# Performance work log

Measured on AMD Instinct MI355X. Metric: run time of the kernel, lower is better.

The kernel has to match this reference:

```python
import jax, jax.numpy as jnp
import numpy as np

B, T, HID = 2, 2048, 1024
NH, HD = 16, 64          # attn_heads, head_size (NH*HD == HID)
FF = 4 * HID
LN_EPS = 1e-5            # torch nn.LayerNorm default


def setup_inputs() -> dict:
    key = jax.random.key(0)
    ks = jax.random.split(key, 14)
    s = lambda fan_in: fan_in ** -0.5
    return {
        "embedding": jax.random.normal(ks[0], (B, T, HID), jnp.float32),
        # per-head q/k/v projections stacked: [HID, NH, HD] (no bias, as in torch code)
        "Wq": jax.random.normal(ks[1], (HID, NH, HD), jnp.float32) * s(HID),
        "Wk": jax.random.normal(ks[2], (HID, NH, HD), jnp.float32) * s(HID),
        "Wv": jax.random.normal(ks[3], (HID, NH, HD), jnp.float32) * s(HID),
        "Wo": jax.random.normal(ks[4], (HID, HID), jnp.float32) * s(HID),
        "W1": jax.random.normal(ks[5], (HID, FF), jnp.float32) * s(HID),
        "b1": jnp.zeros((FF,), jnp.float32),
        "W2": jax.random.normal(ks[6], (FF, HID), jnp.float32) * s(FF),
        "b2": jnp.zeros((HID,), jnp.float32),
        "g1": jnp.ones((HID,), jnp.float32),
        "be1": jnp.zeros((HID,), jnp.float32),
        "g2": jnp.ones((HID,), jnp.float32),
        "be2": jnp.zeros((HID,), jnp.float32),
    }


def _layer_norm(h, g, b):
    mu = jnp.mean(h, axis=-1, keepdims=True)
    var = jnp.mean(jnp.square(h - mu), axis=-1, keepdims=True)
    return (h - mu) * jax.lax.rsqrt(var + LN_EPS) * g + b


def _block(x, Wq, Wk, Wv, Wo, W1, b1, W2, b2, g1, be1, g2, be2):
    # --- causal multi-head self-attention (pre-LN) ---
    h = _layer_norm(x, g1, be1)
    q = jnp.einsum('btd,dhk->bhtk', h, Wq)
    k = jnp.einsum('btd,dhk->bhtk', h, Wk)
    v = jnp.einsum('btd,dhk->bhtk', h, Wv)
    scores = jnp.einsum('bhtk,bhsk->bhts', q, k) * (HD ** -0.5)
    causal = jnp.tril(jnp.ones((T, T), bool))
    scores = jnp.where(causal, scores, -jnp.inf)
    attn = jax.nn.softmax(scores, axis=-1)
    ctx = jnp.einsum('bhts,bhsk->bhtk', attn, v)          # [B,NH,T,HD]
    ctx = ctx.transpose(0, 2, 1, 3).reshape(x.shape[0], x.shape[1], HID)
    x = x + ctx @ Wo
    # --- feed-forward (pre-LN) ---
    h2 = _layer_norm(x, g2, be2)
    ff = jax.nn.relu(h2 @ W1 + b1) @ W2 + b2
    return x + ff


def reference(embedding, Wq, Wk, Wv, Wo, W1, b1, W2, b2, g1, be1, g2, be2):
    return _block(embedding, Wq, Wk, Wv, Wo, W1, b1, W2, b2, g1, be1, g2, be2)
```

## Files before the change

kernel.cpp:

```cpp
#include <hip/hip_runtime.h>
#include <math.h>

#define HIDDEN 1024
#define SEQ    2048
#define NHEAD  16
#define HDIM   64
#define ROWS   (2 * SEQ)

typedef float  floatx4  __attribute__((ext_vector_type(4)));
typedef float  floatx16 __attribute__((ext_vector_type(16)));
typedef __bf16 bf16x8   __attribute__((ext_vector_type(8)));
typedef __bf16 bf16x4   __attribute__((ext_vector_type(4)));

#define AS1(p) ((const __attribute__((address_space(1))) void*)(p))
#define AS3(p) ((__attribute__((address_space(3))) void*)(p))

#define SWZ(row, chunk) ((((chunk) ^ ((row) & 7)) * 8))

__global__ __launch_bounds__(256) void ln_kernel(const float* __restrict__ x,
                                                 const float* __restrict__ g,
                                                 const float* __restrict__ beta,
                                                 __bf16* __restrict__ out) {
    int row = blockIdx.x;
    int tid = threadIdx.x;
    const float* xr = x + (size_t)row * HIDDEN;
    float4 v = *(const float4*)(xr + tid * 4);
    float s  = v.x + v.y + v.z + v.w;
    float s2 = v.x * v.x + v.y * v.y + v.z * v.z + v.w * v.w;
#pragma unroll
    for (int off = 1; off < 64; off <<= 1) {
        s  += __shfl_xor(s, off, 64);
        s2 += __shfl_xor(s2, off, 64);
    }
    __shared__ float red[8];
    int wid = tid >> 6;
    if ((tid & 63) == 0) { red[wid] = s; red[wid + 4] = s2; }
    __syncthreads();
    s  = red[0] + red[1] + red[2] + red[3];
    s2 = red[4] + red[5] + red[6] + red[7];
    float mu  = s * (1.0f / HIDDEN);
    float var = fmaxf(s2 * (1.0f / HIDDEN) - mu * mu, 0.0f);
    float inv = rsqrtf(var + 1e-5f);
    float4 gv = *(const float4*)(g + tid * 4);
    float4 bv = *(const float4*)(beta + tid * 4);
    bf16x4 o;
    o[0] = (__bf16)((v.x - mu) * inv * gv.x + bv.x);
    o[1] = (__bf16)((v.y - mu) * inv * gv.y + bv.y);
    o[2] = (__bf16)((v.z - mu) * inv * gv.z + bv.z);
    o[3] = (__bf16)((v.w - mu) * inv * gv.w + bv.w);
    *(bf16x4*)(out + (size_t)row * HIDDEN + tid * 4) = o;
}

__global__ __launch_bounds__(256) void red_wo_ln(const float* __restrict__ emb,
                                                 const __bf16* __restrict__ p0,
                                                 const __bf16* __restrict__ p1,
                                                 const float* __restrict__ g,
                                                 const float* __restrict__ beta,
                                                 float* __restrict__ out,
                                                 __bf16* __restrict__ h2) {
    int row = blockIdx.x;
    int tid = threadIdx.x;
    size_t i = (size_t)row * HIDDEN + tid * 4;
    float4 e = *(const float4*)(emb + i);
    bf16x4 a = *(const bf16x4*)(p0 + i);
    bf16x4 b = *(const bf16x4*)(p1 + i);
    float4 v;
    v.x = e.x + (float)a[0] + (float)b[0];
    v.y = e.y + (float)a[1] + (float)b[1];
    v.z = e.z + (float)a[2] + (float)b[2];
    v.w = e.w + (float)a[3] + (float)b[3];
    *(float4*)(out + i) = v;

    float s  = v.x + v.y + v.z + v.w;
    float s2 = v.x * v.x + v.y * v.y + v.z * v.z + v.w * v.w;
#pragma unroll
    for (int off = 1; off < 64; off <<= 1) {
        s  += __shfl_xor(s, off, 64);
        s2 += __shfl_xor(s2, off, 64);
    }
    __shared__ float red[8];
    int wid = tid >> 6;
    if ((tid & 63) == 0) { red[wid] = s; red[wid + 4] = s2; }
    __syncthreads();
    s  = red[0] + red[1] + red[2] + red[3];
    s2 = red[4] + red[5] + red[6] + red[7];
    float mu  = s * (1.0f / HIDDEN);
    float var = fmaxf(s2 * (1.0f / HIDDEN) - mu * mu, 0.0f);
    float inv = rsqrtf(var + 1e-5f);
    float4 gv = *(const float4*)(g + tid * 4);
    float4 bv = *(const float4*)(beta + tid * 4);
    bf16x4 o;
    o[0] = (__bf16)((v.x - mu) * inv * gv.x + bv.x);
    o[1] = (__bf16)((v.y - mu) * inv * gv.y + bv.y);
    o[2] = (__bf16)((v.z - mu) * inv * gv.z + bv.z);
    o[3] = (__bf16)((v.w - mu) * inv * gv.w + bv.w);
    *(bf16x4*)(h2 + i) = o;
}

__global__ __launch_bounds__(256) void convt_all(const float* __restrict__ Wq,
                                                 const float* __restrict__ Wk,
                                                 const float* __restrict__ Wv,
                                                 const float* __restrict__ Wo,
                                                 const float* __restrict__ W1,
                                                 const float* __restrict__ W2,
                                                 __bf16* __restrict__ BtQKV,
                                                 __bf16* __restrict__ BtO,
                                                 __bf16* __restrict__ Bt1,
                                                 __bf16* __restrict__ Bt2) {
    __shared__ float t[32][33];
    int id = blockIdx.x;
    const float* in; __bf16* out; int K, N, nt, kt;
    if (id < 4096) {
        int job = id >> 10, tt = id & 1023;
        nt = tt & 31; kt = tt >> 5; K = 1024; N = 1024;
        if (job == 0)      { in = Wq; out = BtQKV; }
        else if (job == 1) { in = Wk; out = BtQKV + 1024 * 1024; }
        else if (job == 2) { in = Wv; out = BtQKV + 2 * 1024 * 1024; }
        else               { in = Wo; out = BtO; }
    } else if (id < 8192) {
        int tt = id - 4096;
        nt = tt & 127; kt = tt >> 7; K = 1024; N = 4096; in = W1; out = Bt1;
    } else {
        int tt = id - 8192;
        nt = tt & 31; kt = tt >> 5; K = 4096; N = 1024; in = W2; out = Bt2;
    }
    int n0 = nt * 32, k0 = kt * 32;
    int r  = threadIdx.x >> 3;
    int c4 = (threadIdx.x & 7) * 4;
    float4 v = *(const float4*)(in + (size_t)(k0 + r) * N + n0 + c4);
    t[r][c4 + 0] = v.x; t[r][c4 + 1] = v.y; t[r][c4 + 2] = v.z; t[r][c4 + 3] = v.w;
    __syncthreads();
    bf16x4 o;
    o[0] = (__bf16)t[c4 + 0][r];
    o[1] = (__bf16)t[c4 + 1][r];
    o[2] = (__bf16)t[c4 + 2][r];
    o[3] = (__bf16)t[c4 + 3][r];
    *(bf16x4*)(out + (size_t)(n0 + r) * K + k0 + c4) = o;
}

__device__ __forceinline__ void mfma_core128(const __bf16* __restrict__ A,
                                             const __bf16* __restrict__ Bt,
                                             int Kstride, int Klen,
                                             int m0, int n0, int tid,
                                             floatx16 (&acc)[2][2]) {
    __shared__ __bf16 As[128 * 32];
    __shared__ __bf16 Bs[128 * 32];
    int lane = tid & 63;
    int wave = tid >> 6;
    int wr = wave >> 1, wc = wave & 1;

    int sr = lane >> 2;
    int sk = 8 * ((lane & 3) ^ ((sr >> 1) & 3));
    const __bf16* ga0 = A  + (size_t)(m0 + wave * 16 + sr) * Kstride + sk;
    const __bf16* ga1 = ga0 + (size_t)64 * Kstride;
    const __bf16* gb0 = Bt + (size_t)(n0 + wave * 16 + sr) * Kstride + sk;
    const __bf16* gb1 = gb0 + (size_t)64 * Kstride;
    __bf16* la0 = &As[wave * 512];
    __bf16* la1 = &As[2048 + wave * 512];
    __bf16* lb0 = &Bs[wave * 512];
    __bf16* lb1 = &Bs[2048 + wave * 512];

    int fm = lane & 31;
    int gswz = (lane >> 1) & 3;
    int slot0 = ((lane >> 5) + 0) ^ gswz;
    int slot1 = ((lane >> 5) + 2) ^ gswz;

    for (int k0 = 0; k0 < Klen; k0 += 32) {
        __builtin_amdgcn_global_load_lds(AS1(ga0 + k0), AS3(la0), 16, 0, 0);
        __builtin_amdgcn_global_load_lds(AS1(ga1 + k0), AS3(la1), 16, 0, 0);
        __builtin_amdgcn_global_load_lds(AS1(gb0 + k0), AS3(lb0), 16, 0, 0);
        __builtin_amdgcn_global_load_lds(AS1(gb1 + k0), AS3(lb1), 16, 0, 0);
        __syncthreads();

        bf16x8 af[2][2], bfv[2][2];
#pragma unroll
        for (int i = 0; i < 2; i++) {
            const __bf16* rp = As + (size_t)(wr * 64 + i * 32 + fm) * 32;
            af[i][0] = *(const bf16x8*)(rp + slot0 * 8);
            af[i][1] = *(const bf16x8*)(rp + slot1 * 8);
        }
#pragma unroll
        for (int j = 0; j < 2; j++) {
            const __bf16* rp = Bs + (size_t)(wc * 64 + j * 32 + fm) * 32;
            bfv[j][0] = *(const bf16x8*)(rp + slot0 * 8);
            bfv[j][1] = *(const bf16x8*)(rp + slot1 * 8);
        }
#pragma unroll
        for (int t = 0; t < 2; t++)
#pragma unroll
            for (int i = 0; i < 2; i++)
#pragma unroll
                for (int j = 0; j < 2; j++)
                    acc[i][j] = __builtin_amdgcn_mfma_f32_32x32x16_bf16(
                        af[i][t], bfv[j][t], acc[i][j], 0, 0, 0);
        __syncthreads();
    }
}

template <typename OutT, bool BIAS, bool RELU, bool RES>
__global__ __launch_bounds__(256) void mgemm(const __bf16* __restrict__ A,
                                             const __bf16* __restrict__ Bt,
                                             const float* __restrict__ bias,
                                             const float* __restrict__ res,
                                             OutT* __restrict__ C,
                                             int M, int N, int Kstride, int Klen) {
    int tid = threadIdx.x;
    int lane = tid & 63;
    int wave = tid >> 6;
    int m0 = blockIdx.x * 128, n0 = blockIdx.y * 128;
    int wr = wave >> 1, wc = wave & 1;
    floatx16 acc[2][2] = {};
    mfma_core128(A, Bt, Kstride, Klen, m0, n0, tid, acc);

#pragma unroll
    for (int i = 0; i < 2; i++) {
#pragma unroll
        for (int j = 0; j < 2; j++) {
            int col  = n0 + wc * 64 + j * 32 + (lane & 31);
            int rowb = m0 + wr * 64 + i * 32 + 4 * (lane >> 5);
#pragma unroll
            for (int reg = 0; reg < 16; reg++) {
                int row = rowb + (reg & 3) + 8 * (reg >> 2);
                float v = acc[i][j][reg];
                if (BIAS) v += bias[col];
                if (RELU) v = fmaxf(v, 0.0f);
                if (RES)  v += res[(size_t)row * N + col];
                C[(size_t)row * N + col] = (OutT)v;
            }
        }
    }
}

__global__ __launch_bounds__(256) void mgemm_sk(const __bf16* __restrict__ A,
                                                const __bf16* __restrict__ Bt,
                                                __bf16* __restrict__ P0,
                                                __bf16* __restrict__ P3,
                                                int M, int N, int Kstride, int Klen) {
    int z = blockIdx.z;
    const __bf16* Az  = A  + (size_t)z * Klen;
    const __bf16* Btz = Bt + (size_t)z * Klen;
    __bf16* C = (z == 3) ? P3 : (P0 + (size_t)z * M * N);

    int tid = threadIdx.x;
    int lane = tid & 63;
    int wave = tid >> 6;
    int m0 = blockIdx.x * 128, n0 = blockIdx.y * 128;
    int wr = wave >> 1, wc = wave & 1;
    floatx16 acc[2][2] = {};
    mfma_core128(Az, Btz, Kstride, Klen, m0, n0, tid, acc);

#pragma unroll
    for (int i = 0; i < 2; i++) {
#pragma unroll
        for (int j = 0; j < 2; j++) {
            int col  = n0 + wc * 64 + j * 32 + (lane & 31);
            int rowb = m0 + wr * 64 + i * 32 + 4 * (lane >> 5);
#pragma unroll
            for (int reg = 0; reg < 16; reg++) {
                int row = rowb + (reg & 3) + 8 * (reg >> 2);
                C[(size_t)row * N + col] = (__bf16)acc[i][j][reg];
            }
        }
    }
}

__global__ __launch_bounds__(256) void red_w2(const __bf16* __restrict__ p0,
                                              const __bf16* __restrict__ p3,
                                              const float* __restrict__ b2,
                                              float* __restrict__ out,
                                              int N) {
    size_t i = ((size_t)blockIdx.x * 256 + threadIdx.x) * 8;
    const size_t MN = (size_t)ROWS * HIDDEN;
    bf16x8 a = *(const bf16x8*)(p0 + i);
    bf16x8 b = *(const bf16x8*)(p0 + MN + i);
    bf16x8 c = *(const bf16x8*)(p0 + 2 * MN + i);
    bf16x8 d = *(const bf16x8*)(p3 + i);
    int col = (int)(i & (size_t)(N - 1));
    float4 bb0 = *(const float4*)(b2 + col);
    float4 bb1 = *(const float4*)(b2 + col + 4);
    float4 o0 = *(const float4*)(out + i);
    float4 o1 = *(const float4*)(out + i + 4);
    o0.x += (float)a[0] + (float)b[0] + (float)c[0] + (float)d[0] + bb0.x;
    o0.y += (float)a[1] + (float)b[1] + (float)c[1] + (float)d[1] + bb0.y;
    o0.z += (float)a[2] + (float)b[2] + (float)c[2] + (float)d[2] + bb0.z;
    o0.w += (float)a[3] + (float)b[3] + (float)c[3] + (float)d[3] + bb0.w;
    o1.x += (float)a[4] + (float)b[4] + (float)c[4] + (float)d[4] + bb1.x;
    o1.y += (float)a[5] + (float)b[5] + (float)c[5] + (float)d[5] + bb1.y;
    o1.z += (float)a[6] + (float)b[6] + (float)c[6] + (float)d[6] + bb1.z;
    o1.w += (float)a[7] + (float)b[7] + (float)c[7] + (float)d[7] + bb1.w;
    *(float4*)(out + i)     = o0;
    *(float4*)(out + i + 4) = o1;
}

__global__ __launch_bounds__(256) void vtrans(const __bf16* __restrict__ qkv,
                                              __bf16* __restrict__ Vt) {
    __shared__ __bf16 t[64 * 64];
    int bh = blockIdx.x, b = bh >> 4, h = bh & 15;
    int t0 = blockIdx.y * 64;
    int tid = threadIdx.x;
    int lt = tid >> 2;
    int ds = (tid & 3) * 16;
    const __bf16* vp = qkv + (size_t)(b * SEQ + t0 + lt) * (3 * HIDDEN)
                     + 2 * HIDDEN + h * HDIM + ds;
    bf16x8 a = *(const bf16x8*)vp;
    bf16x8 c = *(const bf16x8*)(vp + 8);
#pragma unroll
    for (int i = 0; i < 8; i++) {
        int d0 = ds + i, d1 = ds + 8 + i;
        t[d0 * 64 + SWZ(d0, lt >> 3) + (lt & 7)] = a[i];
        t[d1 * 64 + SWZ(d1, lt >> 3) + (lt & 7)] = c[i];
    }
    __syncthreads();
    int dr = tid >> 2;
    int c2 = (tid & 3) * 2;
    bf16x8 o0 = *(const bf16x8*)&t[dr * 64 + SWZ(dr, c2)];
    bf16x8 o1 = *(const bf16x8*)&t[dr * 64 + SWZ(dr, c2 + 1)];
    __bf16* op = Vt + ((size_t)bh * HDIM + dr) * SEQ + t0;
    *(bf16x8*)(op + c2 * 8)     = o0;
    *(bf16x8*)(op + c2 * 8 + 8) = o1;
}

__global__ __launch_bounds__(256) void attn_mfma(const __bf16* __restrict__ qkv,
                                                 const __bf16* __restrict__ Vt,
                                                 __bf16* __restrict__ ctx) {
    __shared__ __bf16 Ks[64 * 64];
    __shared__ __bf16 Vs[64 * 64];
    __shared__ __bf16 Ps[4][16 * 64];
    const int QKVW = 3 * HIDDEN;

    int bh = blockIdx.x;
    int qt = gridDim.y - 1 - blockIdx.y;
    int b = bh >> 4, h = bh & 15;
    int tid = threadIdx.x;
    int lane = tid & 63;
    int w = tid >> 6;
    int m = lane & 15;
    int g = lane >> 4;

    const float QSC = 1.44269504f / 8.0f;
    bf16x8 qf[2];
    {
        const __bf16* Qp = qkv + (size_t)(b * SEQ + qt * 64 + w * 16 + m) * QKVW
                         + h * HDIM + g * 8;
        qf[0] = *(const bf16x8*)(Qp);
        qf[1] = *(const bf16x8*)(Qp + 32);
#pragma unroll
        for (int t = 0; t < 2; t++)
#pragma unroll
            for (int i = 0; i < 8; i++)
                qf[t][i] = (__bf16)((float)qf[t][i] * QSC);
    }

    bf16x8 onesf;
#pragma unroll
    for (int i = 0; i < 8; i++) onesf[i] = (__bf16)1.0f;

    floatx4 oacc[4] = {};
    floatx4 lacc = {};

    int srow = tid >> 2;
    int sc0  = (tid & 3) * 2;
    const __bf16* Kg = qkv + (size_t)(b * SEQ) * QKVW + HIDDEN + h * HDIM;
    const __bf16* Vg = Vt + (size_t)bh * HDIM * SEQ;

    for (int kt = 0; kt <= qt; kt++) {
        __syncthreads();
        {
            const __bf16* kp = Kg + (size_t)(kt * 64 + srow) * QKVW + sc0 * 8;
            bf16x8 k0 = *(const bf16x8*)kp;
            bf16x8 k1 = *(const bf16x8*)(kp + 8);
            const __bf16* vp = Vg + (size_t)srow * SEQ + kt * 64 + sc0 * 8;
            bf16x8 v0 = *(const bf16x8*)vp;
            bf16x8 v1 = *(const bf16x8*)(vp + 8);
            *(bf16x8*)&Ks[srow * 64 + SWZ(srow, sc0)]     = k0;
            *(bf16x8*)&Ks[srow * 64 + SWZ(srow, sc0 + 1)] = k1;
            *(bf16x8*)&Vs[srow * 64 + SWZ(srow, sc0)]     = v0;
            *(bf16x8*)&Vs[srow * 64 + SWZ(srow, sc0 + 1)] = v1;
        }
        __syncthreads();

        floatx4 sacc[4] = {};
#pragma unroll
        for (int j = 0; j < 4; j++) {
#pragma unroll
            for (int t = 0; t < 2; t++) {
                int kr = 16 * j + m;
                bf16x8 kf = *(const bf16x8*)&Ks[kr * 64 + SWZ(kr, g + 4 * t)];
                sacc[j] = __builtin_amdgcn_mfma_f32_16x16x32_bf16(
                    qf[t], kf, sacc[j], 0, 0, 0);
            }
        }

        if (kt == qt) {
            int qlocal = w * 16 + 4 * g;
#pragma unroll
            for (int j = 0; j < 4; j++)
#pragma unroll
                for (int r = 0; r < 4; r++)
                    if (16 * j + m > qlocal + r) sacc[j][r] = -INFINITY;
        }

        __bf16* Pw = &Ps[w][0];
#pragma unroll
        for (int j = 0; j < 4; j++)
#pragma unroll
            for (int r = 0; r < 4; r++) {
                float p = exp2f(sacc[j][r]);
                int row = 4 * g + r;
                int key = 16 * j + m;
                Pw[row * 64 + SWZ(row, key >> 3) + (key & 7)] = (__bf16)p;
            }

#pragma unroll
        for (int t = 0; t < 2; t++) {
            bf16x8 pf = *(const bf16x8*)&Pw[m * 64 + SWZ(m, g + 4 * t)];
            lacc = __builtin_amdgcn_mfma_f32_16x16x32_bf16(pf, onesf, lacc, 0, 0, 0);
#pragma unroll
            for (int jd = 0; jd < 4; jd++) {
                int vr = 16 * jd + m;
                bf16x8 vf = *(const bf16x8*)&Vs[vr * 64 + SWZ(vr, g + 4 * t)];
                oacc[jd] = __builtin_amdgcn_mfma_f32_16x16x32_bf16(
                    pf, vf, oacc[jd], 0, 0, 0);
            }
        }
    }

#pragma unroll
    for (int r = 0; r < 4; r++) {
        float invl = 1.0f / lacc[r];
        int row = qt * 64 + w * 16 + 4 * g + r;
        __bf16* cp = ctx + (size_t)(b * SEQ + row) * HIDDEN + h * HDIM;
#pragma unroll
        for (int jd = 0; jd < 4; jd++)
            cp[16 * jd + m] = (__bf16)(oacc[jd][r] * invl);
    }
}

extern "C" void kernel_launch(void* const* d_in, const int* in_sizes, int n_in,
                              void* d_out, int out_size, void* d_ws, size_t ws_size,
                              hipStream_t stream) {
    (void)in_sizes; (void)n_in; (void)out_size; (void)ws_size;
    const float* emb = (const float*)d_in[0];
    const float* Wq  = (const float*)d_in[1];
    const float* Wk  = (const float*)d_in[2];
    const float* Wv  = (const float*)d_in[3];
    const float* Wo  = (const float*)d_in[4];
    const float* W1  = (const float*)d_in[5];
    const float* b1  = (const float*)d_in[6];
    const float* W2  = (const float*)d_in[7];
    const float* b2  = (const float*)d_in[8];
    const float* g1  = (const float*)d_in[9];
    const float* be1 = (const float*)d_in[10];
    const float* g2  = (const float*)d_in[11];
    const float* be2 = (const float*)d_in[12];
    float* out = (float*)d_out;

    __bf16* wsb = (__bf16*)d_ws;
    const size_t ME = 1024 * 1024;
    __bf16* h     = wsb;
    __bf16* qkv   = wsb + 4 * ME;
    __bf16* ctx   = wsb;
    __bf16* ff1   = wsb;
    __bf16* h2    = wsb + 16 * ME;
    __bf16* BtQKV = wsb + 20 * ME;
    __bf16* BtO   = wsb + 23 * ME;
    __bf16* Bt1   = wsb + 24 * ME;
    __bf16* Bt2   = wsb + 28 * ME;
    __bf16* Vt    = wsb + 32 * ME;
    __bf16* woP   = wsb + 4 * ME;
    __bf16* w2P0  = wsb + 16 * ME;
    __bf16* w2P3  = wsb + 32 * ME;

    convt_all<<<12288, 256, 0, stream>>>(Wq, Wk, Wv, Wo, W1, W2,
                                         BtQKV, BtO, Bt1, Bt2);

    ln_kernel<<<ROWS, 256, 0, stream>>>(emb, g1, be1, h);

    mgemm<__bf16, false, false, false><<<dim3(32, 24), 256, 0, stream>>>(
        h, BtQKV, nullptr, nullptr, qkv, ROWS, 3072, 1024, 1024);

    vtrans<<<dim3(32, 32), 256, 0, stream>>>(qkv, Vt);

    attn_mfma<<<dim3(32, 32), 256, 0, stream>>>(qkv, Vt, ctx);

    mgemm_sk<<<dim3(32, 8, 2), 256, 0, stream>>>(
        ctx, BtO, woP, nullptr, ROWS, 1024, 1024, 512);
    red_wo_ln<<<ROWS, 256, 0, stream>>>(emb, woP, woP + 4 * ME, g2, be2, out, h2);

    mgemm<__bf16, true, true, false><<<dim3(32, 32), 256, 0, stream>>>(
        h2, Bt1, b1, nullptr, ff1, ROWS, 4096, 1024, 1024);

    mgemm_sk<<<dim3(32, 8, 4), 256, 0, stream>>>(
        ff1, Bt2, w2P0, w2P3, ROWS, 1024, 4096, 1024);
    red_w2<<<2048, 256, 0, stream>>>(w2P0, w2P3, b2, out, 1024);
}
```

Before: 357.2 us.

## Fuse prep kernels, double-buffer GEMM LDS, fuse V transpose, prefetch attention tiles

Merges the weight convert/transpose and first LayerNorm into one launch. Double-buffers the shared GEMM mainloop so the next K tile's global-to-LDS load overlaps the current MFMAs, with one barrier per iteration instead of two. Writes V transposed straight from the QKV GEMM epilogue, removing the separate vtrans kernel, and has attention register-prefetch the next K/V tile. The trade-offs are twice the LDS use in the GEMM (lower occupancy) and strided small stores for the V columns.

```diff
diff --git a/kernel.cpp b/kernel.cpp
--- a/kernel.cpp
+++ b/kernel.cpp
@@ -17,38 +17,80 @@
 
 #define SWZ(row, chunk) ((((chunk) ^ ((row) & 7)) * 8))
 
-__global__ __launch_bounds__(256) void ln_kernel(const float* __restrict__ x,
-                                                 const float* __restrict__ g,
-                                                 const float* __restrict__ beta,
-                                                 __bf16* __restrict__ out) {
-    int row = blockIdx.x;
+__global__ __launch_bounds__(256) void prep_all(const float* __restrict__ Wq,
+                                                const float* __restrict__ Wk,
+                                                const float* __restrict__ Wv,
+                                                const float* __restrict__ Wo,
+                                                const float* __restrict__ W1,
+                                                const float* __restrict__ W2,
+                                                __bf16* __restrict__ BtQKV,
+                                                __bf16* __restrict__ BtO,
+                                                __bf16* __restrict__ Bt1,
+                                                __bf16* __restrict__ Bt2,
+                                                const float* __restrict__ emb,
+                                                const float* __restrict__ g1,
+                                                const float* __restrict__ be1,
+                                                __bf16* __restrict__ h) {
+    int id = blockIdx.x;
     int tid = threadIdx.x;
-    const float* xr = x + (size_t)row * HIDDEN;
-    float4 v = *(const float4*)(xr + tid * 4);
-    float s  = v.x + v.y + v.z + v.w;
-    float s2 = v.x * v.x + v.y * v.y + v.z * v.z + v.w * v.w;
-#pragma unroll
-    for (int off = 1; off < 64; off <<= 1) {
-        s  += __shfl_xor(s, off, 64);
-        s2 += __shfl_xor(s2, off, 64);
-    }
-    __shared__ float red[8];
-    int wid = tid >> 6;
-    if ((tid & 63) == 0) { red[wid] = s; red[wid + 4] = s2; }
+    if (id >= 12288) {
+        int row = id - 12288;
+        const float* xr = emb + (size_t)row * HIDDEN;
+        float4 v = *(const float4*)(xr + tid * 4);
+        float s  = v.x + v.y + v.z + v.w;
+        float s2 = v.x * v.x + v.y * v.y + v.z * v.z + v.w * v.w;
+#pragma unroll
+        for (int off = 1; off < 64; off <<= 1) {
+            s  += __shfl_xor(s, off, 64);
+            s2 += __shfl_xor(s2, off, 64);
+        }
+        __shared__ float red[8];
+        int wid = tid >> 6;
+        if ((tid & 63) == 0) { red[wid] = s; red[wid + 4] = s2; }
+        __syncthreads();
+        s  = red[0] + red[1] + red[2] + red[3];
+        s2 = red[4] + red[5] + red[6] + red[7];
+        float mu  = s * (1.0f / HIDDEN);
+        float var = fmaxf(s2 * (1.0f / HIDDEN) - mu * mu, 0.0f);
+        float inv = rsqrtf(var + 1e-5f);
+        float4 gv = *(const float4*)(g1 + tid * 4);
+        float4 bv = *(const float4*)(be1 + tid * 4);
+        bf16x4 o;
+        o[0] = (__bf16)((v.x - mu) * inv * gv.x + bv.x);
+        o[1] = (__bf16)((v.y - mu) * inv * gv.y + bv.y);
+        o[2] = (__bf16)((v.z - mu) * inv * gv.z + bv.z);
+        o[3] = (__bf16)((v.w - mu) * inv * gv.w + bv.w);
+        *(bf16x4*)(h + (size_t)row * HIDDEN + tid * 4) = o;
+        return;
+    }
+    __shared__ float t[32][33];
+    const float* in; __bf16* out; int K, N, nt, kt;
+    if (id < 4096) {
+        int job = id >> 10, tt = id & 1023;
+        nt = tt & 31; kt = tt >> 5; K = 1024; N = 1024;
+        if (job == 0)      { in = Wq; out = BtQKV; }
+        else if (job == 1) { in = Wk; out = BtQKV + 1024 * 1024; }
+        else if (job == 2) { in = Wv; out = BtQKV + 2 * 1024 * 1024; }
+        else               { in = Wo; out = BtO; }
+    } else if (id < 8192) {
+        int tt = id - 4096;
+        nt = tt & 127; kt = tt >> 7; K = 1024; N = 4096; in = W1; out = Bt1;
+    } else {
+        int tt = id - 8192;
+        nt = tt & 31; kt = tt >> 5; K = 4096; N = 1024; in = W2; out = Bt2;
+    }
+    int n0 = nt * 32, k0 = kt * 32;
+    int r  = tid >> 3;
+    int c4 = (tid & 7) * 4;
+    float4 v = *(const float4*)(in + (size_t)(k0 + r) * N + n0 + c4);
+    t[r][c4 + 0] = v.x; t[r][c4 + 1] = v.y; t[r][c4 + 2] = v.z; t[r][c4 + 3] = v.w;
     __syncthreads();
-    s  = red[0] + red[1] + red[2] + red[3];
-    s2 = red[4] + red[5] + red[6] + red[7];
-    float mu  = s * (1.0f / HIDDEN);
-    float var = fmaxf(s2 * (1.0f / HIDDEN) - mu * mu, 0.0f);
-    float inv = rsqrtf(var + 1e-5f);
-    float4 gv = *(const float4*)(g + tid * 4);
-    float4 bv = *(const float4*)(beta + tid * 4);
     bf16x4 o;
-    o[0] = (__bf16)((v.x - mu) * inv * gv.x + bv.x);
-    o[1] = (__bf16)((v.y - mu) * inv * gv.y + bv.y);
-    o[2] = (__bf16)((v.z - mu) * inv * gv.z + bv.z);
-    o[3] = (__bf16)((v.w - mu) * inv * gv.w + bv.w);
-    *(bf16x4*)(out + (size_t)row * HIDDEN + tid * 4) = o;
+    o[0] = (__bf16)t[c4 + 0][r];
+    o[1] = (__bf16)t[c4 + 1][r];
+    o[2] = (__bf16)t[c4 + 2][r];
+    o[3] = (__bf16)t[c4 + 3][r];
+    *(bf16x4*)(out + (size_t)(n0 + r) * K + k0 + c4) = o;
 }
 
 __global__ __launch_bounds__(256) void red_wo_ln(const float* __restrict__ emb,
@@ -97,54 +139,14 @@
     *(bf16x4*)(h2 + i) = o;
 }
 
-__global__ __launch_bounds__(256) void convt_all(const float* __restrict__ Wq,
-                                                 const float* __restrict__ Wk,
-                                                 const float* __restrict__ Wv,
-                                                 const float* __restrict__ Wo,
-                                                 const float* __restrict__ W1,
-                                                 const float* __restrict__ W2,
-                                                 __bf16* __restrict__ BtQKV,
-                                                 __bf16* __restrict__ BtO,
-                                                 __bf16* __restrict__ Bt1,
-                                                 __bf16* __restrict__ Bt2) {
-    __shared__ float t[32][33];
-    int id = blockIdx.x;
-    const float* in; __bf16* out; int K, N, nt, kt;
-    if (id < 4096) {
-        int job = id >> 10, tt = id & 1023;
-        nt = tt & 31; kt = tt >> 5; K = 1024; N = 1024;
-        if (job == 0)      { in = Wq; out = BtQKV; }
-        else if (job == 1) { in = Wk; out = BtQKV + 1024 * 1024; }
-        else if (job == 2) { in = Wv; out = BtQKV + 2 * 1024 * 1024; }
-        else               { in = Wo; out = BtO; }
-    } else if (id < 8192) {
-        int tt = id - 4096;
-        nt = tt & 127; kt = tt >> 7; K = 1024; N = 4096; in = W1; out = Bt1;
-    } else {
-        int tt = id - 8192;
-        nt = tt & 31; kt = tt >> 5; K = 4096; N = 1024; in = W2; out = Bt2;
-    }
-    int n0 = nt * 32, k0 = kt * 32;
-    int r  = threadIdx.x >> 3;
-    int c4 = (threadIdx.x & 7) * 4;
-    float4 v = *(const float4*)(in + (size_t)(k0 + r) * N + n0 + c4);
-    t[r][c4 + 0] = v.x; t[r][c4 + 1] = v.y; t[r][c4 + 2] = v.z; t[r][c4 + 3] = v.w;
-    __syncthreads();
-    bf16x4 o;
-    o[0] = (__bf16)t[c4 + 0][r];
-    o[1] = (__bf16)t[c4 + 1][r];
-    o[2] = (__bf16)t[c4 + 2][r];
-    o[3] = (__bf16)t[c4 + 3][r];
-    *(bf16x4*)(out + (size_t)(n0 + r) * K + k0 + c4) = o;
-}
-
 __device__ __forceinline__ void mfma_core128(const __bf16* __restrict__ A,
                                              const __bf16* __restrict__ Bt,
                                              int Kstride, int Klen,
                                              int m0, int n0, int tid,
                                              floatx16 (&acc)[2][2]) {
-    __shared__ __bf16 As[128 * 32];
-    __shared__ __bf16 Bs[128 * 32];
+    __shared__ __bf16 As[2 * 128 * 32];
+    __shared__ __bf16 Bs[2 * 128 * 32];
+    const int BUF = 128 * 32;
     int lane = tid & 63;
     int wave = tid >> 6;
     int wr = wave >> 1, wc = wave & 1;
@@ -165,23 +167,34 @@
     int slot0 = ((lane >> 5) + 0) ^ gswz;
     int slot1 = ((lane >> 5) + 2) ^ gswz;
 
-    for (int k0 = 0; k0 < Klen; k0 += 32) {
-        __builtin_amdgcn_global_load_lds(AS1(ga0 + k0), AS3(la0), 16, 0, 0);
-        __builtin_amdgcn_global_load_lds(AS1(ga1 + k0), AS3(la1), 16, 0, 0);
-        __builtin_amdgcn_global_load_lds(AS1(gb0 + k0), AS3(lb0), 16, 0, 0);
-        __builtin_amdgcn_global_load_lds(AS1(gb1 + k0), AS3(lb1), 16, 0, 0);
+    __builtin_amdgcn_global_load_lds(AS1(ga0), AS3(la0), 16, 0, 0);
+    __builtin_amdgcn_global_load_lds(AS1(ga1), AS3(la1), 16, 0, 0);
+    __builtin_amdgcn_global_load_lds(AS1(gb0), AS3(lb0), 16, 0, 0);
+    __builtin_amdgcn_global_load_lds(AS1(gb1), AS3(lb1), 16, 0, 0);
+
+    int buf = 0;
+    for (int k0 = 0; k0 < Klen; k0 += 32, buf ^= 1) {
         __syncthreads();
+        if (k0 + 32 < Klen) {
+            int nb = (buf ^ 1) * BUF;
+            __builtin_amdgcn_global_load_lds(AS1(ga0 + k0 + 32), AS3(la0 + nb), 16, 0, 0);
+            __builtin_amdgcn_global_load_lds(AS1(ga1 + k0 + 32), AS3(la1 + nb), 16, 0, 0);
+            __builtin_amdgcn_global_load_lds(AS1(gb0 + k0 + 32), AS3(lb0 + nb), 16, 0, 0);
+            __builtin_amdgcn_global_load_lds(AS1(gb1 + k0 + 32), AS3(lb1 + nb), 16, 0, 0);
+        }
+        const __bf16* Ab = As + buf * BUF;
+        const __bf16* Bb = Bs + buf * BUF;
 
         bf16x8 af[2][2], bfv[2][2];
 #pragma unroll
         for (int i = 0; i < 2; i++) {
-            const __bf16* rp = As + (size_t)(wr * 64 + i * 32 + fm) * 32;
+            const __bf16* rp = Ab + (size_t)(wr * 64 + i * 32 + fm) * 32;
             af[i][0] = *(const bf16x8*)(rp + slot0 * 8);
             af[i][1] = *(const bf16x8*)(rp + slot1 * 8);
         }
 #pragma unroll
         for (int j = 0; j < 2; j++) {
-            const __bf16* rp = Bs + (size_t)(wc * 64 + j * 32 + fm) * 32;
+            const __bf16* rp = Bb + (size_t)(wc * 64 + j * 32 + fm) * 32;
             bfv[j][0] = *(const bf16x8*)(rp + slot0 * 8);
             bfv[j][1] = *(const bf16x8*)(rp + slot1 * 8);
         }
@@ -193,7 +206,6 @@
                 for (int j = 0; j < 2; j++)
                     acc[i][j] = __builtin_amdgcn_mfma_f32_32x32x16_bf16(
                         af[i][t], bfv[j][t], acc[i][j], 0, 0, 0);
-        __syncthreads();
     }
 }
 
@@ -226,6 +238,51 @@
                 if (RELU) v = fmaxf(v, 0.0f);
                 if (RES)  v += res[(size_t)row * N + col];
                 C[(size_t)row * N + col] = (OutT)v;
+            }
+        }
+    }
+}
+
+__global__ __launch_bounds__(256) void mgemm_qkv(const __bf16* __restrict__ A,
+                                                 const __bf16* __restrict__ Bt,
+                                                 __bf16* __restrict__ C,
+                                                 __bf16* __restrict__ Vt) {
+    const int N = 3072;
+    int tid = threadIdx.x;
+    int lane = tid & 63;
+    int wave = tid >> 6;
+    int m0 = blockIdx.x * 128, n0 = blockIdx.y * 128;
+    int wr = wave >> 1, wc = wave & 1;
+    floatx16 acc[2][2] = {};
+    mfma_core128(A, Bt, 1024, 1024, m0, n0, tid, acc);
+
+#pragma unroll
+    for (int i = 0; i < 2; i++) {
+#pragma unroll
+        for (int j = 0; j < 2; j++) {
+            int col  = n0 + wc * 64 + j * 32 + (lane & 31);
+            int rowb = m0 + wr * 64 + i * 32 + 4 * (lane >> 5);
+            if (col < 2048) {
+#pragma unroll
+                for (int reg = 0; reg < 16; reg++) {
+                    int row = rowb + (reg & 3) + 8 * (reg >> 2);
+                    C[(size_t)row * N + col] = (__bf16)acc[i][j][reg];
+                }
+            } else {
+                int vcol = col - 2048;
+                int hh = vcol >> 6, dd = vcol & 63;
+#pragma unroll
+                for (int rq = 0; rq < 4; rq++) {
+                    int row0 = rowb + 8 * rq;
+                    int bb = row0 >> 11;
+                    int tt = row0 & 2047;
+                    bf16x4 pack;
+                    pack[0] = (__bf16)acc[i][j][4 * rq + 0];
+                    pack[1] = (__bf16)acc[i][j][4 * rq + 1];
+                    pack[2] = (__bf16)acc[i][j][4 * rq + 2];
+                    pack[3] = (__bf16)acc[i][j][4 * rq + 3];
+                    *(bf16x4*)&Vt[(((size_t)bb * 16 + hh) * 64 + dd) * SEQ + tt] = pack;
+                }
             }
         }
     }
@@ -292,34 +349,6 @@
     *(float4*)(out + i + 4) = o1;
 }
 
-__global__ __launch_bounds__(256) void vtrans(const __bf16* __restrict__ qkv,
-                                              __bf16* __restrict__ Vt) {
-    __shared__ __bf16 t[64 * 64];
-    int bh = blockIdx.x, b = bh >> 4, h = bh & 15;
-    int t0 = blockIdx.y * 64;
-    int tid = threadIdx.x;
-    int lt = tid >> 2;
-    int ds = (tid & 3) * 16;
-    const __bf16* vp = qkv + (size_t)(b * SEQ + t0 + lt) * (3 * HIDDEN)
-                     + 2 * HIDDEN + h * HDIM + ds;
-    bf16x8 a = *(const bf16x8*)vp;
-    bf16x8 c = *(const bf16x8*)(vp + 8);
-#pragma unroll
-    for (int i = 0; i < 8; i++) {
-        int d0 = ds + i, d1 = ds + 8 + i;
-        t[d0 * 64 + SWZ(d0, lt >> 3) + (lt & 7)] = a[i];
-        t[d1 * 64 + SWZ(d1, lt >> 3) + (lt & 7)] = c[i];
-    }
-    __syncthreads();
-    int dr = tid >> 2;
-    int c2 = (tid & 3) * 2;
-    bf16x8 o0 = *(const bf16x8*)&t[dr * 64 + SWZ(dr, c2)];
-    bf16x8 o1 = *(const bf16x8*)&t[dr * 64 + SWZ(dr, c2 + 1)];
-    __bf16* op = Vt + ((size_t)bh * HDIM + dr) * SEQ + t0;
-    *(bf16x8*)(op + c2 * 8)     = o0;
-    *(bf16x8*)(op + c2 * 8 + 8) = o1;
-}
-
 __global__ __launch_bounds__(256) void attn_mfma(const __bf16* __restrict__ qkv,
                                                  const __bf16* __restrict__ Vt,
                                                  __bf16* __restrict__ ctx) {
@@ -363,21 +392,32 @@
     const __bf16* Kg = qkv + (size_t)(b * SEQ) * QKVW + HIDDEN + h * HDIM;
     const __bf16* Vg = Vt + (size_t)bh * HDIM * SEQ;
 
+    bf16x8 pk0, pk1, pv0, pv1;
+    {
+        const __bf16* kp = Kg + (size_t)srow * QKVW + sc0 * 8;
+        pk0 = *(const bf16x8*)kp;
+        pk1 = *(const bf16x8*)(kp + 8);
+        const __bf16* vp = Vg + (size_t)srow * SEQ + sc0 * 8;
+        pv0 = *(const bf16x8*)vp;
+        pv1 = *(const bf16x8*)(vp + 8);
+    }
+
     for (int kt = 0; kt <= qt; kt++) {
         __syncthreads();
-        {
-            const __bf16* kp = Kg + (size_t)(kt * 64 + srow) * QKVW + sc0 * 8;
-            bf16x8 k0 = *(const bf16x8*)kp;
-            bf16x8 k1 = *(const bf16x8*)(kp + 8);
-            const __bf16* vp = Vg + (size_t)srow * SEQ + kt * 64 + sc0 * 8;
-            bf16x8 v0 = *(const bf16x8*)vp;
-            bf16x8 v1 = *(const bf16x8*)(vp + 8);
-            *(bf16x8*)&Ks[srow * 64 + SWZ(srow, sc0)]     = k0;
-            *(bf16x8*)&Ks[srow * 64 + SWZ(srow, sc0 + 1)] = k1;
-            *(bf16x8*)&Vs[srow * 64 + SWZ(srow, sc0)]     = v0;
-            *(bf16x8*)&Vs[srow * 64 + SWZ(srow, sc0 + 1)] = v1;
-        }
+        *(bf16x8*)&Ks[srow * 64 + SWZ(srow, sc0)]     = pk0;
+        *(bf16x8*)&Ks[srow * 64 + SWZ(srow, sc0 + 1)] = pk1;
+        *(bf16x8*)&Vs[srow * 64 + SWZ(srow, sc0)]     = pv0;
+        *(bf16x8*)&Vs[srow * 64 + SWZ(srow, sc0 + 1)] = pv1;
         __syncthreads();
+
+        if (kt < qt) {
+            const __bf16* kp = Kg + (size_t)((kt + 1) * 64 + srow) * QKVW + sc0 * 8;
+            pk0 = *(const bf16x8*)kp;
+            pk1 = *(const bf16x8*)(kp + 8);
+            const __bf16* vp = Vg + (size_t)srow * SEQ + (kt + 1) * 64 + sc0 * 8;
+            pv0 = *(const bf16x8*)vp;
+            pv1 = *(const bf16x8*)(vp + 8);
+        }
 
         floatx4 sacc[4] = {};
 #pragma unroll
@@ -471,15 +511,11 @@
     __bf16* w2P0  = wsb + 16 * ME;
     __bf16* w2P3  = wsb + 32 * ME;
 
-    convt_all<<<12288, 256, 0, stream>>>(Wq, Wk, Wv, Wo, W1, W2,
-                                         BtQKV, BtO, Bt1, Bt2);
-
-    ln_kernel<<<ROWS, 256, 0, stream>>>(emb, g1, be1, h);
-
-    mgemm<__bf16, false, false, false><<<dim3(32, 24), 256, 0, stream>>>(
-        h, BtQKV, nullptr, nullptr, qkv, ROWS, 3072, 1024, 1024);
-
-    vtrans<<<dim3(32, 32), 256, 0, stream>>>(qkv, Vt);
+    prep_all<<<16384, 256, 0, stream>>>(Wq, Wk, Wv, Wo, W1, W2,
+                                        BtQKV, BtO, Bt1, Bt2,
+                                        emb, g1, be1, h);
+
+    mgemm_qkv<<<dim3(32, 24), 256, 0, stream>>>(h, BtQKV, qkv, Vt);
 
     attn_mfma<<<dim3(32, 32), 256, 0, stream>>>(qkv, Vt, ctx);
 
```

Result: faster. 345.1 us (-3.4%).
